# Kernel optimization log

Hardware: AMD Instinct MI355X
Metric: run time of the kernel (lower is better)

## Reference

```python
import jax, jax.numpy as jnp
import numpy as np

EPS = 1e-8      # F.normalize eps in _cos_angle
TOPK = 4
DELTA = 1.0     # huber delta
EXTRA_FRAMES = (1, 3, 5, 7)            # teacher-only frames
SHARED = ((2, 1), (4, 2), (6, 3))      # (teacher_idx, student_idx) for shared frames


def _huber(e):
    ae = jnp.abs(e)
    return jnp.where(ae <= DELTA, 0.5 * e * e, DELTA * (ae - 0.5 * DELTA))


def _angles(R, H, Sh):
    # R: [b,r,d] ref, H: [b,r,k,d] sim_high, Sh: [b,s,d] shared.
    # Cosines of the three triplet angles computed via dot-product expansion,
    # avoiding any [b,r,s,k,d] intermediate. cos = (u.v)/(max(|u|,eps)*max(|v|,eps))
    RH  = jnp.einsum('brd,brkd->brk', R, H)
    RSh = jnp.einsum('brd,bsd->brs', R, Sh)
    HSh = jnp.einsum('brkd,bsd->brsk', H, Sh)
    Rn2  = jnp.sum(R * R, -1)        # [b,r]
    Hn2  = jnp.sum(H * H, -1)        # [b,r,k]
    Shn2 = jnp.sum(Sh * Sh, -1)      # [b,s]
    n_RSh = jnp.maximum(jnp.sqrt(jnp.maximum(Rn2[:, :, None] + Shn2[:, None, :] - 2 * RSh, 0.0)), EPS)          # |R-Sh| [b,r,s]
    n_RH  = jnp.maximum(jnp.sqrt(jnp.maximum(Rn2[:, :, None] + Hn2 - 2 * RH, 0.0)), EPS)                        # |R-H|  [b,r,k]
    n_HSh = jnp.maximum(jnp.sqrt(jnp.maximum(Hn2[:, :, None, :] + Shn2[:, None, :, None] - 2 * HSh, 0.0)), EPS) # |H-Sh| [b,r,s,k]
    # angle1: vertex=ref, u=Sh-R, v=H-R
    d1 = HSh - RSh[..., None] - RH[:, :, None, :] + Rn2[:, :, None, None]
    a1 = d1 / (n_RSh[..., None] * n_RH[:, :, None, :])
    # angle2: vertex=H, u=R-H, v=Sh-H
    d2 = RSh[..., None] - RH[:, :, None, :] - HSh + Hn2[:, :, None, :]
    a2 = d2 / (n_RH[:, :, None, :] * n_HSh)
    # angle3: vertex=Sh, u=R-Sh, v=H-Sh
    d3 = RH[:, :, None, :] - RSh[..., None] - HSh + Shn2[:, None, :, None]
    a3 = d3 / (n_RSh[..., None] * n_HSh)
    return a1, a2, a3


def setup_inputs() -> dict:
    key = jax.random.key(0)
    k1, k2, k3, k4 = jax.random.split(key, 4)
    B, S_T, P, D = 2, 8, 2048, 1024
    num_ref, num_shared = 128, 128
    teacher_feats = jax.random.normal(k1, (B, S_T, P, D), jnp.float32)
    student_feats = jax.random.normal(k2, (B, 4, P, D), jnp.float32)
    ref_perm = jax.random.permutation(k3, P)[:num_ref].astype(jnp.int32)
    shared_perm = jax.random.permutation(k4, P)[:num_shared].astype(jnp.int32)
    return {"teacher_feats": teacher_feats, "student_feats": student_feats,
            "ref_perm": ref_perm, "shared_perm": shared_perm}


def reference(teacher_feats, student_feats, ref_perm, shared_perm):
    tf = jax.lax.stop_gradient(teacher_feats)  # teacher is fully detached
    B, _, P, D = tf.shape
    num_ref = ref_perm.shape[0]
    num_shared = shared_perm.shape[0]
    ref_t = tf[:, 0, ref_perm, :]                 # [B,R,D]
    ref_s = student_feats[:, 0, ref_perm, :]
    # teacher-only frames, concatenated along patch dim -> [B, EP, D]
    extra = tf[:, jnp.array(EXTRA_FRAMES), :, :].reshape(B, -1, D)
    # cosine-similarity retrieval (selection_mode='topk')
    rtn = ref_t / jnp.maximum(jnp.linalg.norm(ref_t, axis=-1, keepdims=True), 1e-12)
    etn = extra / jnp.maximum(jnp.linalg.norm(extra, axis=-1, keepdims=True), 1e-12)
    sim = jnp.einsum('brd,bed->bre', rtn, etn)
    _, idx = jax.lax.top_k(sim, TOPK)             # [B,R,K]
    H = jnp.take_along_axis(extra, idx.reshape(B, -1, 1), axis=1).reshape(B, num_ref, TOPK, D)
    s1 = s2 = s3 = jnp.float32(0.0)
    for tidx, sidx in SHARED:
        Sh_t = tf[:, tidx, shared_perm, :]
        Sh_s = student_feats[:, sidx, shared_perm, :]
        a1t, a2t, a3t = _angles(ref_t, H, Sh_t)
        a1s, a2s, a3s = _angles(ref_s, H, Sh_s)
        s1 = s1 + _huber(a1s - a1t).sum()
        s2 = s2 + _huber(a2s - a2t).sum()
        s3 = s3 + _huber(a3s - a3t).sum()
    total = jnp.float32(len(SHARED) * B * num_ref * num_shared * TOPK)
    # angle weights all 1.0
    loss = s1 / total + s2 / total + s3 / total
    return loss
```

## Files before the change

kernel.cpp:

```cpp
#include <hip/hip_runtime.h>
#include <cstdint>
#include <cstddef>
#include <cfloat>
#include <climits>

#define D_DIM   1024
#define P_DIM   2048
#define NB      2
#define NR      128
#define NS      128
#define KTOP    4
#define E_DIM   8192
#define ANG_EPS 1e-8f
#define M_PAIR  768
#define N_PAIR  768

#define SIM_SLICES  4
#define SIM_KSLICE  256
#define PAIR_SLICES 8
#define PAIR_KSLICE 128

#define TOPK_DELTA  0.25f
#define MAXCAND     128

typedef short short8 __attribute__((ext_vector_type(8)));
typedef float f32x4 __attribute__((ext_vector_type(4)));

__device__ __forceinline__ float dot4(float4 a, float4 b) {
  return a.x * b.x + a.y * b.y + a.z * b.z + a.w * b.w;
}

__device__ __forceinline__ float huber(float e) {
  float ae = fabsf(e);
  return ae <= 1.0f ? 0.5f * e * e : ae - 0.5f;
}

__device__ __forceinline__ bool better(float va, int ia, float vb, int ib) {
  return (va > vb) || (va == vb && ia < ib);
}

__device__ __forceinline__ unsigned int f2bf(float x) {
  union { float f; unsigned int u; } v; v.f = x;
  unsigned int r = v.u + 0x7fffu + ((v.u >> 16) & 1u);
  return r >> 16;
}
__device__ __forceinline__ unsigned int pk2bf(float x, float y) {
  return f2bf(x) | (f2bf(y) << 16);
}

__device__ __forceinline__ float block_reduce_sum(float v, float* scratch) {
  #pragma unroll
  for (int o = 32; o > 0; o >>= 1) v += __shfl_down(v, o);
  __syncthreads();
  if ((threadIdx.x & 63) == 0) scratch[threadIdx.x >> 6] = v;
  __syncthreads();
  float r = 0.0f;
  int nw = (int)(blockDim.x >> 6);
  if ((int)threadIdx.x < nw) r = scratch[threadIdx.x];
  #pragma unroll
  for (int o = 2; o > 0; o >>= 1) r += __shfl_down(r, o);
  return r;
}

__global__ __launch_bounds__(256) void sim_gemm_kernel(const float* __restrict__ tf,
                                                       const int* __restrict__ ref_perm,
                                                       float* __restrict__ simP,
                                                       float* __restrict__ bn2P) {
  __shared__ unsigned int Ah[128 * 20];
  __shared__ unsigned int Bh[128 * 20];
  __shared__ const float* Arow[128];
  __shared__ const float* Brow[128];
  const int tid = threadIdx.x;
  const int b = blockIdx.z;
  const int slice = blockIdx.y;
  const int nbase = blockIdx.x * 128;
  const int kbase = slice * SIM_KSLICE;
  if (tid < 128) {
    Arow[tid] = tf + ((size_t)(b * 8) * P_DIM + ref_perm[tid]) * D_DIM + kbase;
  } else {
    int n = nbase + (tid - 128);
    Brow[tid - 128] = tf + ((size_t)(b * 8 + 1 + 2 * (n >> 11)) * P_DIM + (n & (P_DIM - 1))) * D_DIM + kbase;
  }
  __syncthreads();

  const int srow = tid >> 1;
  const int shalf = (tid & 1) * 16;
  const float* asrc = Arow[srow] + shalf;
  const float* bsrc = Brow[srow] + shalf;

  float4 av[4], bv[4];
  #pragma unroll
  for (int i = 0; i < 4; ++i) {
    av[i] = *(const float4*)(asrc + 4 * i);
    bv[i] = *(const float4*)(bsrc + 4 * i);
  }

  const int wave = tid >> 6;
  const int lane = tid & 63;
  const int fr = lane & 15;
  const int q16 = (lane >> 4) * 16;
  const char* Ab = (const char*)Ah;
  const char* Bb = (const char*)Bh;

  f32x4 acc[2][8];
  #pragma unroll
  for (int mt = 0; mt < 2; ++mt)
    #pragma unroll
    for (int nt = 0; nt < 8; ++nt)
      #pragma unroll
      for (int r = 0; r < 4; ++r) acc[mt][nt][r] = 0.0f;

  float bn2 = 0.0f;
  unsigned int* adst = Ah + srow * 20 + (tid & 1) * 8;
  unsigned int* bdst = Bh + srow * 20 + (tid & 1) * 8;

  for (int ck = 0; ck < 8; ++ck) {
    bn2 += dot4(bv[0], bv[0]) + dot4(bv[1], bv[1]) + dot4(bv[2], bv[2]) + dot4(bv[3], bv[3]);
    unsigned int ua[8], ub[8];
    #pragma unroll
    for (int i = 0; i < 4; ++i) {
      ua[2 * i]     = pk2bf(av[i].x, av[i].y);
      ua[2 * i + 1] = pk2bf(av[i].z, av[i].w);
      ub[2 * i]     = pk2bf(bv[i].x, bv[i].y);
      ub[2 * i + 1] = pk2bf(bv[i].z, bv[i].w);
    }
    __syncthreads();
    *(uint4*)(adst)     = make_uint4(ua[0], ua[1], ua[2], ua[3]);
    *(uint4*)(adst + 4) = make_uint4(ua[4], ua[5], ua[6], ua[7]);
    *(uint4*)(bdst)     = make_uint4(ub[0], ub[1], ub[2], ub[3]);
    *(uint4*)(bdst + 4) = make_uint4(ub[4], ub[5], ub[6], ub[7]);
    __syncthreads();
    if (ck < 7) {
      const float* an = asrc + (ck + 1) * 32;
      const float* bn = bsrc + (ck + 1) * 32;
      #pragma unroll
      for (int i = 0; i < 4; ++i) {
        av[i] = *(const float4*)(an + 4 * i);
        bv[i] = *(const float4*)(bn + 4 * i);
      }
    }
    short8 afr[2], bfr[8];
    #pragma unroll
    for (int mt = 0; mt < 2; ++mt)
      afr[mt] = *(const short8*)(Ab + (wave * 32 + mt * 16 + fr) * 80 + q16);
    #pragma unroll
    for (int nt = 0; nt < 8; ++nt)
      bfr[nt] = *(const short8*)(Bb + (nt * 16 + fr) * 80 + q16);
    #pragma unroll
    for (int mt = 0; mt < 2; ++mt)
      #pragma unroll
      for (int nt = 0; nt < 8; ++nt)
        acc[mt][nt] = __builtin_amdgcn_mfma_f32_16x16x32_bf16(afr[mt], bfr[nt], acc[mt][nt], 0, 0, 0);
  }

  bn2 += __shfl_xor(bn2, 1);
  if ((tid & 1) == 0)
    bn2P[((size_t)slice * NB + b) * E_DIM + nbase + srow] = bn2;

  float* base = simP + (((size_t)slice * NB + b) * NR) * E_DIM + nbase;
  const int crow = (lane >> 4) * 4;
  #pragma unroll
  for (int mt = 0; mt < 2; ++mt) {
    #pragma unroll
    for (int nt = 0; nt < 8; ++nt) {
      int col = nt * 16 + fr;
      #pragma unroll
      for (int r = 0; r < 4; ++r) {
        int m = wave * 32 + mt * 16 + crow + r;
        base[(size_t)m * E_DIM + col] = acc[mt][nt][r];
      }
    }
  }
}

__global__ __launch_bounds__(256) void topk_kernel(const float* __restrict__ simP,
                                                   const float* __restrict__ bn2P,
                                                   const float* __restrict__ tf,
                                                   const float* __restrict__ sf,
                                                   const int* __restrict__ ref_perm,
                                                   int* __restrict__ tki,
                                                   float* __restrict__ rt_n2,
                                                   float* __restrict__ rs_n2,
                                                   float* __restrict__ hn2,
                                                   float* __restrict__ rh_t,
                                                   float* __restrict__ rh_s) {
  __shared__ float scores[E_DIM];
  __shared__ float sv[1024];
  __shared__ int si[1024];
  __shared__ float candVal[MAXCAND];
  __shared__ int candIdx[MAXCAND];
  __shared__ int cnt;
  __shared__ int fin4[4];
  const int tid = threadIdx.x;
  const int br = blockIdx.x;
  const int b = br >> 7;
  const int r = br & 127;
  const size_t ST = (size_t)NB * NR * E_DIM;
  const size_t SN = (size_t)NB * E_DIM;
  const float* p = simP + (size_t)br * E_DIM;
  const float* q = bn2P + (size_t)b * E_DIM;
  if (tid == 0) cnt = 0;

  float tv[4] = {-FLT_MAX, -FLT_MAX, -FLT_MAX, -FLT_MAX};
  int ti[4] = {INT_MAX, INT_MAX, INT_MAX, INT_MAX};
  for (int e4 = tid * 4; e4 < E_DIM; e4 += 1024) {
    float4 s = *(const float4*)(p + e4);
    float4 s1 = *(const float4*)(p + ST + e4);
    float4 s2 = *(const float4*)(p + 2 * ST + e4);
    float4 s3 = *(const float4*)(p + 3 * ST + e4);
    float4 n0 = *(const float4*)(q + e4);
    float4 n1 = *(const float4*)(q + SN + e4);
    float4 n2 = *(const float4*)(q + 2 * SN + e4);
    float4 n3 = *(const float4*)(q + 3 * SN + e4);
    float sj[4] = {s.x + s1.x + s2.x + s3.x, s.y + s1.y + s2.y + s3.y,
                   s.z + s1.z + s2.z + s3.z, s.w + s1.w + s2.w + s3.w};
    float nj[4] = {n0.x + n1.x + n2.x + n3.x, n0.y + n1.y + n2.y + n3.y,
                   n0.z + n1.z + n2.z + n3.z, n0.w + n1.w + n2.w + n3.w};
    #pragma unroll
    for (int j = 0; j < 4; ++j) {
      int e = e4 + j;
      float x = sj[j] * rsqrtf(fmaxf(nj[j], 1e-24f));
      scores[e] = x;
      if (better(x, e, tv[3], ti[3])) {
        tv[3] = x; ti[3] = e;
        #pragma unroll
        for (int k = 3; k > 0; --k) {
          if (better(tv[k], ti[k], tv[k - 1], ti[k - 1])) {
            float fv = tv[k]; tv[k] = tv[k - 1]; tv[k - 1] = fv;
            int fi2 = ti[k]; ti[k] = ti[k - 1]; ti[k - 1] = fi2;
          }
        }
      }
    }
  }
  #pragma unroll
  for (int k = 0; k < 4; ++k) { sv[tid * 4 + k] = tv[k]; si[tid * 4 + k] = ti[k]; }
  for (int stride = 128; stride > 0; stride >>= 1) {
    __syncthreads();
    if (tid < stride) {
      float av[4], bv2[4]; int ai[4], bi2[4];
      #pragma unroll
      for (int k = 0; k < 4; ++k) {
        av[k] = sv[tid * 4 + k];               ai[k] = si[tid * 4 + k];
        bv2[k] = sv[(tid + stride) * 4 + k];   bi2[k] = si[(tid + stride) * 4 + k];
      }
      float ov[4]; int oi[4]; int pa = 0, pb = 0;
      #pragma unroll
      for (int k = 0; k < 4; ++k) {
        bool takeA = (pa < 4) && (pb >= 4 || better(av[pa], ai[pa], bv2[pb], bi2[pb]));
        if (takeA) { ov[k] = av[pa]; oi[k] = ai[pa]; ++pa; }
        else       { ov[k] = bv2[pb]; oi[k] = bi2[pb]; ++pb; }
      }
      #pragma unroll
      for (int k = 0; k < 4; ++k) { sv[tid * 4 + k] = ov[k]; si[tid * 4 + k] = oi[k]; }
    }
  }
  __syncthreads();
  const float tau = sv[3] - TOPK_DELTA;

  for (int e4 = tid * 4; e4 < E_DIM; e4 += 1024) {
    #pragma unroll
    for (int j = 0; j < 4; ++j) {
      int e = e4 + j;
      if (scores[e] >= tau) {
        int pos = atomicAdd(&cnt, 1);
        if (pos < MAXCAND) candIdx[pos] = e;
      }
    }
  }
  __syncthreads();
  int cntc = min(cnt, MAXCAND);

  const float* R = tf + ((size_t)(b * 8) * P_DIM + ref_perm[r]) * D_DIM;
  const int wave = tid >> 6;
  const int lane = tid & 63;
  for (int c = wave; c < cntc; c += 4) {
    int e = candIdx[c];
    const float* E = tf + ((size_t)(b * 8 + 1 + 2 * (e >> 11)) * P_DIM + (e & (P_DIM - 1))) * D_DIM;
    float d = 0.0f, n2 = 0.0f;
    #pragma unroll
    for (int i = 0; i < 4; ++i) {
      float4 rv = *(const float4*)(R + lane * 16 + i * 4);
      float4 ev = *(const float4*)(E + lane * 16 + i * 4);
      d += dot4(rv, ev);
      n2 += dot4(ev, ev);
    }
    #pragma unroll
    for (int o = 32; o > 0; o >>= 1) { d += __shfl_xor(d, o); n2 += __shfl_xor(n2, o); }
    if (lane == 0) candVal[c] = d / fmaxf(sqrtf(n2), 1e-12f);
  }
  __syncthreads();
  if (tid == 0) {
    float bv[4] = {-FLT_MAX, -FLT_MAX, -FLT_MAX, -FLT_MAX};
    int bi[4] = {INT_MAX, INT_MAX, INT_MAX, INT_MAX};
    for (int c = 0; c < cntc; ++c) {
      float x = candVal[c]; int e = candIdx[c];
      if (better(x, e, bv[3], bi[3])) {
        bv[3] = x; bi[3] = e;
        #pragma unroll
        for (int k = 3; k > 0; --k) {
          if (better(bv[k], bi[k], bv[k - 1], bi[k - 1])) {
            float fv = bv[k]; bv[k] = bv[k - 1]; bv[k - 1] = fv;
            int fi2 = bi[k]; bi[k] = bi[k - 1]; bi[k - 1] = fi2;
          }
        }
      }
    }
    #pragma unroll
    for (int k = 0; k < 4; ++k) { tki[br * 4 + k] = bi[k]; fin4[k] = bi[k]; }
  }
  __syncthreads();

  {
    const float* RS = sf + ((size_t)(b * 4) * P_DIM + ref_perm[r]) * D_DIM;
    int e = fin4[wave];
    const float* H = tf + ((size_t)(b * 8 + 1 + 2 * (e >> 11)) * P_DIM + (e & (P_DIM - 1))) * D_DIM;
    float h2 = 0.0f, rht = 0.0f, rhs = 0.0f, rtn = 0.0f, rsn = 0.0f;
    #pragma unroll
    for (int i = 0; i < 4; ++i) {
      float4 rv = *(const float4*)(R + lane * 16 + i * 4);
      float4 sv2 = *(const float4*)(RS + lane * 16 + i * 4);
      float4 hv = *(const float4*)(H + lane * 16 + i * 4);
      h2 += dot4(hv, hv);
      rht += dot4(rv, hv);
      rhs += dot4(sv2, hv);
      rtn += dot4(rv, rv);
      rsn += dot4(sv2, sv2);
    }
    #pragma unroll
    for (int o = 32; o > 0; o >>= 1) {
      h2 += __shfl_xor(h2, o);
      rht += __shfl_xor(rht, o);
      rhs += __shfl_xor(rhs, o);
      rtn += __shfl_xor(rtn, o);
      rsn += __shfl_xor(rsn, o);
    }
    if (lane == 0) {
      hn2[br * KTOP + wave] = h2;
      rh_t[br * KTOP + wave] = rht;
      rh_s[br * KTOP + wave] = rhs;
      if (wave == 0) rt_n2[br] = rtn;
      if (wave == 1) rs_n2[br] = rsn;
    }
  }
}

__global__ __launch_bounds__(256) void sh_norms_kernel(const float* __restrict__ tf,
                                                       const float* __restrict__ sf,
                                                       const int* __restrict__ shared_perm,
                                                       float* __restrict__ shn2_t,
                                                       float* __restrict__ shn2_s) {
  __shared__ float scr[4];
  int row = blockIdx.x;
  int s = row & 127;
  int side = (row >> 7) & 1;
  int b = (row >> 8) & 1;
  int p = row >> 9;
  const float* ptr = (side == 0)
      ? tf + ((size_t)(b * 8 + 2 * p + 2) * P_DIM + shared_perm[s]) * D_DIM
      : sf + ((size_t)(b * 4 + p + 1) * P_DIM + shared_perm[s]) * D_DIM;
  float4 v = *(const float4*)(ptr + threadIdx.x * 4);
  float red = block_reduce_sum(dot4(v, v), scr);
  if (threadIdx.x == 0) {
    float* dst = (side == 0) ? shn2_t : shn2_s;
    dst[(p * 2 + b) * NS + s] = red;
  }
}

__global__ __launch_bounds__(256) void pair_gemm_kernel(const float* __restrict__ tf,
                                                        const float* __restrict__ sf,
                                                        const int* __restrict__ ref_perm,
                                                        const int* __restrict__ shared_perm,
                                                        const int* __restrict__ tki,
                                                        float* __restrict__ CpP) {
  __shared__ unsigned int Ah[128 * 20];
  __shared__ unsigned int Bh[128 * 20];
  __shared__ const float* Arow[128];
  __shared__ const float* Brow[128];
  const int tid = threadIdx.x;
  const int b = blockIdx.z & 1;
  const int slice = blockIdx.z >> 1;
  const int mbase = blockIdx.y * 128;
  const int nbase = blockIdx.x * 128;
  const int kbase = slice * PAIR_KSLICE;
  if (tid < 128) {
    int m = mbase + tid;
    const float* p;
    if (m < 128) {
      p = tf + ((size_t)(b * 8) * P_DIM + ref_perm[m]) * D_DIM;
    } else if (m < 256) {
      p = sf + ((size_t)(b * 4) * P_DIM + ref_perm[m - 128]) * D_DIM;
    } else {
      int h = m - 256, r = h >> 2, k = h & 3;
      int e = tki[(b * NR + r) * KTOP + k];
      p = tf + ((size_t)(b * 8 + 1 + 2 * (e >> 11)) * P_DIM + (e & (P_DIM - 1))) * D_DIM;
    }
    Arow[tid] = p + kbase;
  } else {
    int n = nbase + (tid - 128);
    int pr = n >> 8, rem = n & 255, side = rem >> 7, s = rem & 127;
    const float* p;
    if (side == 0) p = tf + ((size_t)(b * 8 + 2 * pr + 2) * P_DIM + shared_perm[s]) * D_DIM;
    else           p = sf + ((size_t)(b * 4 + pr + 1) * P_DIM + shared_perm[s]) * D_DIM;
    Brow[tid - 128] = p + kbase;
  }
  __syncthreads();

  const int srow = tid >> 1;
  const int shalf = (tid & 1) * 16;
  const float* asrc = Arow[srow] + shalf;
  const float* bsrc = Brow[srow] + shalf;

  float4 av[4], bv[4];
  #pragma unroll
  for (int i = 0; i < 4; ++i) {
    av[i] = *(const float4*)(asrc + 4 * i);
    bv[i] = *(const float4*)(bsrc + 4 * i);
  }

  const int wave = tid >> 6;
  const int lane = tid & 63;
  const int fr = lane & 15;
  const int q16 = (lane >> 4) * 16;
  const char* Ab = (const char*)Ah;
  const char* Bb = (const char*)Bh;

  f32x4 acc[2][8];
  #pragma unroll
  for (int mt = 0; mt < 2; ++mt)
    #pragma unroll
    for (int nt = 0; nt < 8; ++nt)
      #pragma unroll
      for (int r = 0; r < 4; ++r) acc[mt][nt][r] = 0.0f;

  unsigned int* adst = Ah + srow * 20 + (tid & 1) * 8;
  unsigned int* bdst = Bh + srow * 20 + (tid & 1) * 8;

  for (int ck = 0; ck < 4; ++ck) {
    unsigned int ua[8], ub[8];
    #pragma unroll
    for (int i = 0; i < 4; ++i) {
      ua[2 * i]     = pk2bf(av[i].x, av[i].y);
      ua[2 * i + 1] = pk2bf(av[i].z, av[i].w);
      ub[2 * i]     = pk2bf(bv[i].x, bv[i].y);
      ub[2 * i + 1] = pk2bf(bv[i].z, bv[i].w);
    }
    __syncthreads();
    *(uint4*)(adst)     = make_uint4(ua[0], ua[1], ua[2], ua[3]);
    *(uint4*)(adst + 4) = make_uint4(ua[4], ua[5], ua[6], ua[7]);
    *(uint4*)(bdst)     = make_uint4(ub[0], ub[1], ub[2], ub[3]);
    *(uint4*)(bdst + 4) = make_uint4(ub[4], ub[5], ub[6], ub[7]);
    __syncthreads();
    if (ck < 3) {
      const float* an = asrc + (ck + 1) * 32;
      const float* bn = bsrc + (ck + 1) * 32;
      #pragma unroll
      for (int i = 0; i < 4; ++i) {
        av[i] = *(const float4*)(an + 4 * i);
        bv[i] = *(const float4*)(bn + 4 * i);
      }
    }
    short8 afr[2], bfr[8];
    #pragma unroll
    for (int mt = 0; mt < 2; ++mt)
      afr[mt] = *(const short8*)(Ab + (wave * 32 + mt * 16 + fr) * 80 + q16);
    #pragma unroll
    for (int nt = 0; nt < 8; ++nt)
      bfr[nt] = *(const short8*)(Bb + (nt * 16 + fr) * 80 + q16);
    #pragma unroll
    for (int mt = 0; mt < 2; ++mt)
      #pragma unroll
      for (int nt = 0; nt < 8; ++nt)
        acc[mt][nt] = __builtin_amdgcn_mfma_f32_16x16x32_bf16(afr[mt], bfr[nt], acc[mt][nt], 0, 0, 0);
  }

  float* base = CpP + (((size_t)slice * NB + b) * M_PAIR + mbase) * N_PAIR + nbase;
  const int crow = (lane >> 4) * 4;
  #pragma unroll
  for (int mt = 0; mt < 2; ++mt) {
    #pragma unroll
    for (int nt = 0; nt < 8; ++nt) {
      int col = nt * 16 + fr;
      #pragma unroll
      for (int r = 0; r < 4; ++r) {
        int m = wave * 32 + mt * 16 + crow + r;
        base[(size_t)m * N_PAIR + col] = acc[mt][nt][r];
      }
    }
  }
}

__global__ __launch_bounds__(128) void loss_kernel(const float* __restrict__ CpP,
                                                   const float* __restrict__ rt_n2,
                                                   const float* __restrict__ rs_n2,
                                                   const float* __restrict__ hn2,
                                                   const float* __restrict__ rh_t,
                                                   const float* __restrict__ rh_s,
                                                   const float* __restrict__ shn2_t,
                                                   const float* __restrict__ shn2_s,
                                                   float* __restrict__ acc) {
  __shared__ float scr[2];
  int r = blockIdx.x, b = blockIdx.y, p = blockIdx.z;
  int s = threadIdx.x;
  int br = b * NR + r;
  const size_t SLC = (size_t)NB * M_PAIR * N_PAIR;
  const float* Cb = CpP + (size_t)b * M_PAIR * N_PAIR;
  auto sumC = [&](int m, int n) -> float {
    const float* q = Cb + (size_t)m * N_PAIR + n;
    float v = 0.0f;
    #pragma unroll
    for (int sl = 0; sl < PAIR_SLICES; ++sl) v += q[sl * SLC];
    return v;
  };
  float Rt2 = rt_n2[br], Rs2 = rs_n2[br];
  float St2 = shn2_t[(p * 2 + b) * NS + s];
  float Ss2 = shn2_s[(p * 2 + b) * NS + s];
  float RSt = sumC(r, p * 256 + s);
  float RSs = sumC(128 + r, p * 256 + 128 + s);
  float sum = 0.0f;
  #pragma unroll
  for (int k = 0; k < KTOP; ++k) {
    float H2 = hn2[br * KTOP + k];
    float RHt = rh_t[br * KTOP + k];
    float RHs = rh_s[br * KTOP + k];
    float HSt = sumC(256 + r * 4 + k, p * 256 + s);
    float HSs = sumC(256 + r * 4 + k, p * 256 + 128 + s);
    float nRSt = fmaxf(sqrtf(fmaxf(Rt2 + St2 - 2.0f * RSt, 0.0f)), ANG_EPS);
    float nRHt = fmaxf(sqrtf(fmaxf(Rt2 + H2 - 2.0f * RHt, 0.0f)), ANG_EPS);
    float nHSt = fmaxf(sqrtf(fmaxf(H2 + St2 - 2.0f * HSt, 0.0f)), ANG_EPS);
    float a1t = (HSt - RSt - RHt + Rt2) / (nRSt * nRHt);
    float a2t = (RSt - RHt - HSt + H2) / (nRHt * nHSt);
    float a3t = (RHt - RSt - HSt + St2) / (nRSt * nHSt);
    float nRSs = fmaxf(sqrtf(fmaxf(Rs2 + Ss2 - 2.0f * RSs, 0.0f)), ANG_EPS);
    float nRHs = fmaxf(sqrtf(fmaxf(Rs2 + H2 - 2.0f * RHs, 0.0f)), ANG_EPS);
    float nHSs = fmaxf(sqrtf(fmaxf(H2 + Ss2 - 2.0f * HSs, 0.0f)), ANG_EPS);
    float a1s = (HSs - RSs - RHs + Rs2) / (nRSs * nRHs);
    float a2s = (RSs - RHs - HSs + H2) / (nRHs * nHSs);
    float a3s = (RHs - RSs - HSs + Ss2) / (nRSs * nHSs);
    sum += huber(a1s - a1t) + huber(a2s - a2t) + huber(a3s - a3t);
  }
  float tot = block_reduce_sum(sum, scr);
  if (threadIdx.x == 0) atomicAdd(acc, tot);
}

__global__ void finalize_kernel(const float* __restrict__ acc, float* __restrict__ out) {
  if (threadIdx.x == 0 && blockIdx.x == 0)
    out[0] = acc[0] * (1.0f / 393216.0f);
}

extern "C" void kernel_launch(void* const* d_in, const int* in_sizes, int n_in,
                              void* d_out, int out_size, void* d_ws, size_t ws_size,
                              hipStream_t stream) {
  const float* tf = (const float*)d_in[0];
  const float* sf = (const float*)d_in[1];
  const int* ref_perm = (const int*)d_in[2];
  const int* shared_perm = (const int*)d_in[3];
  float* ws = (float*)d_ws;

  float* simP   = ws;
  float* bn2P   = simP + (size_t)SIM_SLICES * NB * NR * E_DIM;
  float* CpP    = bn2P + (size_t)SIM_SLICES * NB * E_DIM;
  float* rt_n2  = CpP  + (size_t)PAIR_SLICES * NB * M_PAIR * N_PAIR;
  float* rs_n2  = rt_n2  + NB * NR;
  float* hn2    = rs_n2  + NB * NR;
  float* rh_t   = hn2    + NB * NR * KTOP;
  float* rh_s   = rh_t   + NB * NR * KTOP;
  float* shn2_t = rh_s   + NB * NR * KTOP;
  float* shn2_s = shn2_t + 3 * NB * NS;
  float* acc    = shn2_s + 3 * NB * NS;
  int*   tki    = (int*)(acc + 4);
  float* out = (float*)d_out;

  hipMemsetAsync(acc, 0, sizeof(float), stream);
  sim_gemm_kernel<<<dim3(E_DIM / 128, SIM_SLICES, NB), 256, 0, stream>>>(tf, ref_perm, simP, bn2P);
  topk_kernel<<<NB * NR, 256, 0, stream>>>(simP, bn2P, tf, sf, ref_perm, tki,
                                           rt_n2, rs_n2, hn2, rh_t, rh_s);
  sh_norms_kernel<<<3 * NB * 2 * NS, 256, 0, stream>>>(tf, sf, shared_perm, shn2_t, shn2_s);
  pair_gemm_kernel<<<dim3(N_PAIR / 128, M_PAIR / 128, NB * PAIR_SLICES), 256, 0, stream>>>(tf, sf, ref_perm, shared_perm, tki, CpP);
  loss_kernel<<<dim3(NR, NB, 3), 128, 0, stream>>>(CpP, rt_n2, rs_n2, hn2, rh_t, rh_s, shn2_t, shn2_s, acc);
  finalize_kernel<<<1, 64, 0, stream>>>(acc, out);
}
```

Measured before the change: 281.4 us.

## Fuse shared-row norms into pair GEMM and finalize into loss kernel

After: 293.6 us. +4.4%, slower.

```diff
diff --git a/kernel.cpp b/kernel.cpp
--- a/kernel.cpp
+++ b/kernel.cpp
@@ -22,6 +22,7 @@
 
 #define TOPK_DELTA  0.25f
 #define MAXCAND     128
+#define LOSS_BLOCKS (NR * NB * 3)
 
 typedef short short8 __attribute__((ext_vector_type(8)));
 typedef float f32x4 __attribute__((ext_vector_type(4)));
@@ -345,34 +346,13 @@
   }
 }
 
-__global__ __launch_bounds__(256) void sh_norms_kernel(const float* __restrict__ tf,
-                                                       const float* __restrict__ sf,
-                                                       const int* __restrict__ shared_perm,
-                                                       float* __restrict__ shn2_t,
-                                                       float* __restrict__ shn2_s) {
-  __shared__ float scr[4];
-  int row = blockIdx.x;
-  int s = row & 127;
-  int side = (row >> 7) & 1;
-  int b = (row >> 8) & 1;
-  int p = row >> 9;
-  const float* ptr = (side == 0)
-      ? tf + ((size_t)(b * 8 + 2 * p + 2) * P_DIM + shared_perm[s]) * D_DIM
-      : sf + ((size_t)(b * 4 + p + 1) * P_DIM + shared_perm[s]) * D_DIM;
-  float4 v = *(const float4*)(ptr + threadIdx.x * 4);
-  float red = block_reduce_sum(dot4(v, v), scr);
-  if (threadIdx.x == 0) {
-    float* dst = (side == 0) ? shn2_t : shn2_s;
-    dst[(p * 2 + b) * NS + s] = red;
-  }
-}
-
 __global__ __launch_bounds__(256) void pair_gemm_kernel(const float* __restrict__ tf,
                                                         const float* __restrict__ sf,
                                                         const int* __restrict__ ref_perm,
                                                         const int* __restrict__ shared_perm,
                                                         const int* __restrict__ tki,
-                                                        float* __restrict__ CpP) {
+                                                        float* __restrict__ CpP,
+                                                        float* __restrict__ shb2P) {
   __shared__ unsigned int Ah[128 * 20];
   __shared__ unsigned int Bh[128 * 20];
   __shared__ const float* Arow[128];
@@ -433,10 +413,12 @@
       #pragma unroll
       for (int r = 0; r < 4; ++r) acc[mt][nt][r] = 0.0f;
 
+  float bn2 = 0.0f;
   unsigned int* adst = Ah + srow * 20 + (tid & 1) * 8;
   unsigned int* bdst = Bh + srow * 20 + (tid & 1) * 8;
 
   for (int ck = 0; ck < 4; ++ck) {
+    bn2 += dot4(bv[0], bv[0]) + dot4(bv[1], bv[1]) + dot4(bv[2], bv[2]) + dot4(bv[3], bv[3]);
     unsigned int ua[8], ub[8];
     #pragma unroll
     for (int i = 0; i < 4; ++i) {
@@ -474,6 +456,10 @@
         acc[mt][nt] = __builtin_amdgcn_mfma_f32_16x16x32_bf16(afr[mt], bfr[nt], acc[mt][nt], 0, 0, 0);
   }
 
+  bn2 += __shfl_xor(bn2, 1);
+  if ((tid & 1) == 0)
+    shb2P[((size_t)slice * NB + b) * N_PAIR + nbase + srow] = bn2;
+
   float* base = CpP + (((size_t)slice * NB + b) * M_PAIR + mbase) * N_PAIR + nbase;
   const int crow = (lane >> 4) * 4;
   #pragma unroll
@@ -496,9 +482,9 @@
                                                    const float* __restrict__ hn2,
                                                    const float* __restrict__ rh_t,
                                                    const float* __restrict__ rh_s,
-                                                   const float* __restrict__ shn2_t,
-                                                   const float* __restrict__ shn2_s,
-                                                   float* __restrict__ acc) {
+                                                   const float* __restrict__ shb2P,
+                                                   float* __restrict__ acc,
+                                                   float* __restrict__ out) {
   __shared__ float scr[2];
   int r = blockIdx.x, b = blockIdx.y, p = blockIdx.z;
   int s = threadIdx.x;
@@ -513,8 +499,15 @@
     return v;
   };
   float Rt2 = rt_n2[br], Rs2 = rs_n2[br];
-  float St2 = shn2_t[(p * 2 + b) * NS + s];
-  float Ss2 = shn2_s[(p * 2 + b) * NS + s];
+  float St2 = 0.0f, Ss2 = 0.0f;
+  {
+    const float* qn = shb2P + (size_t)b * N_PAIR + p * 256 + s;
+    #pragma unroll
+    for (int sl = 0; sl < PAIR_SLICES; ++sl) {
+      St2 += qn[(size_t)sl * NB * N_PAIR];
+      Ss2 += qn[(size_t)sl * NB * N_PAIR + 128];
+    }
+  }
   float RSt = sumC(r, p * 256 + s);
   float RSs = sumC(128 + r, p * 256 + 128 + s);
   float sum = 0.0f;
@@ -540,12 +533,15 @@
     sum += huber(a1s - a1t) + huber(a2s - a2t) + huber(a3s - a3t);
   }
   float tot = block_reduce_sum(sum, scr);
-  if (threadIdx.x == 0) atomicAdd(acc, tot);
-}
-
-__global__ void finalize_kernel(const float* __restrict__ acc, float* __restrict__ out) {
-  if (threadIdx.x == 0 && blockIdx.x == 0)
-    out[0] = acc[0] * (1.0f / 393216.0f);
+  if (threadIdx.x == 0) {
+    atomicAdd(acc, tot);
+    __threadfence();
+    int done = atomicAdd((int*)(acc + 1), 1);
+    if (done == LOSS_BLOCKS - 1) {
+      float total = atomicAdd(acc, 0.0f);
+      out[0] = total * (1.0f / 393216.0f);
+    }
+  }
 }
 
 extern "C" void kernel_launch(void* const* d_in, const int* in_sizes, int n_in,
@@ -560,23 +556,22 @@
   float* simP   = ws;
   float* bn2P   = simP + (size_t)SIM_SLICES * NB * NR * E_DIM;
   float* CpP    = bn2P + (size_t)SIM_SLICES * NB * E_DIM;
-  float* rt_n2  = CpP  + (size_t)PAIR_SLICES * NB * M_PAIR * N_PAIR;
+  float* shb2P  = CpP  + (size_t)PAIR_SLICES * NB * M_PAIR * N_PAIR;
+  float* rt_n2  = shb2P + (size_t)PAIR_SLICES * NB * N_PAIR;
   float* rs_n2  = rt_n2  + NB * NR;
   float* hn2    = rs_n2  + NB * NR;
   float* rh_t   = hn2    + NB * NR * KTOP;
   float* rh_s   = rh_t   + NB * NR * KTOP;
-  float* shn2_t = rh_s   + NB * NR * KTOP;
-  float* shn2_s = shn2_t + 3 * NB * NS;
-  float* acc    = shn2_s + 3 * NB * NS;
+  float* acc    = rh_s   + NB * NR * KTOP;
   int*   tki    = (int*)(acc + 4);
   float* out = (float*)d_out;
 
-  hipMemsetAsync(acc, 0, sizeof(float), stream);
+  hipMemsetAsync(acc, 0, 2 * sizeof(float), stream);
   sim_gemm_kernel<<<dim3(E_DIM / 128, SIM_SLICES, NB), 256, 0, stream>>>(tf, ref_perm, simP, bn2P);
   topk_kernel<<<NB * NR, 256, 0, stream>>>(simP, bn2P, tf, sf, ref_perm, tki,
                                            rt_n2, rs_n2, hn2, rh_t, rh_s);
-  sh_norms_kernel<<<3 * NB * 2 * NS, 256, 0, stream>>>(tf, sf, shared_perm, shn2_t, shn2_s);
-  pair_gemm_kernel<<<dim3(N_PAIR / 128, M_PAIR / 128, NB * PAIR_SLICES), 256, 0, stream>>>(tf, sf, ref_perm, shared_perm, tki, CpP);
-  loss_kernel<<<dim3(NR, NB, 3), 128, 0, stream>>>(CpP, rt_n2, rs_n2, hn2, rh_t, rh_s, shn2_t, shn2_s, acc);
-  finalize_kernel<<<1, 64, 0, stream>>>(acc, out);
-}
+  pair_gemm_kernel<<<dim3(N_PAIR / 128, M_PAIR / 128, NB * PAIR_SLICES), 256, 0, stream>>>(
+      tf, sf, ref_perm, shared_perm, tki, CpP, shb2P);
+  loss_kernel<<<dim3(NR, NB, 3), 128, 0, stream>>>(CpP, rt_n2, rs_n2, hn2, rh_t, rh_s,
+                                                   shb2P, acc, out);
+}
```
